# Performance work log

Measured on AMD Instinct MI355X. Metric: run time of the kernel, lower is better.

## Reference

```python
import jax, jax.numpy as jnp
import numpy as np

B = 16384
N_TABLES = 26
N_ROWS = 100000
D = 64


def _mlp(x, params, last_sigmoid=False):
    n = len(params)
    for i, (w, b) in enumerate(params):
        x = x @ w.T + b
        if last_sigmoid and i == n - 1:
            x = jax.nn.sigmoid(x)
        else:
            x = jax.nn.relu(x)
    return x


def setup_inputs() -> dict:
    key = jax.random.key(0)
    ks = jax.random.split(key, 16)

    def glorot(k, m, n):
        return jax.random.normal(k, (m, n), jnp.float32) * np.sqrt(2.0 / (m + n))

    def bias(k, m):
        return jax.random.normal(k, (m,), jnp.float32) * np.sqrt(1.0 / m)

    return {
        "dense_x": jax.random.normal(ks[0], (B, 13), jnp.float32),
        "lS_i": jax.random.randint(ks[1], (N_TABLES, B), 0, N_ROWS, jnp.int64 if jax.config.jax_enable_x64 else jnp.int32),
        "emb_W": jax.random.normal(ks[2], (N_TABLES, N_ROWS, D), jnp.float32) * np.sqrt(1.0 / N_ROWS),
        "bot_w0": glorot(ks[3], 512, 13), "bot_b0": bias(ks[4], 512),
        "bot_w1": glorot(ks[5], 256, 512), "bot_b1": bias(ks[6], 256),
        "bot_w2": glorot(ks[7], 64, 256), "bot_b2": bias(ks[8], 64),
        "top_w0": glorot(ks[9], 512, 415), "top_b0": bias(ks[10], 512),
        "top_w1": glorot(ks[11], 256, 512), "top_b1": bias(ks[12], 256),
        "top_w2": glorot(ks[13], 1, 256), "top_b2": bias(ks[14], 1),
    }


def reference(dense_x, lS_i, emb_W, bot_w0, bot_b0, bot_w1, bot_b1, bot_w2, bot_b2,
              top_w0, top_b0, top_w1, top_b1, top_w2, top_b2):
    # bottom MLP: [B,13] -> [B,64]
    x = _mlp(dense_x, [(bot_w0, bot_b0), (bot_w1, bot_b1), (bot_w2, bot_b2)])

    # embedding lookups: one index per sample per table (EmbeddingBag sum over bag of 1)
    # emb_W: [T, N, D], lS_i: [T, B] -> ly: [T, B, D]
    ly = jnp.take_along_axis(emb_W, lS_i[:, :, None], axis=1)  # [T, B, D]

    # interaction: T = concat(x, ly) -> [B, 27, D]; Z = T T^T; lower-tri (i>j) flatten
    T = jnp.concatenate([x[None], ly], axis=0).transpose(1, 0, 2)  # [B, 27, D]
    Z = jnp.einsum("bnd,bmd->bnm", T, T)  # [B, 27, 27]
    li, lj = jnp.tril_indices(N_TABLES + 1, k=-1)  # same order as torch list comp
    Zflat = Z[:, li, lj]  # [B, 351]
    R = jnp.concatenate([x, Zflat], axis=1)  # [B, 415]

    # top MLP with sigmoid output
    p = _mlp(R, [(top_w0, top_b0), (top_w1, top_b1), (top_w2, top_b2)], last_sigmoid=True)
    return p
```

## Files before the change

kernel.cpp:

```cpp
#include <hip/hip_runtime.h>
#include <math.h>


#define BATCH 16384
#define NTAB 26
#define NF 27
#define NROWS 100000
#define EDIM 64
#define PAIRS 351
#define RLD 416

typedef __attribute__((ext_vector_type(4))) float   accfrag_t;
typedef __attribute__((ext_vector_type(8))) short   bfrag_t;
typedef __attribute__((ext_vector_type(4))) unsigned short u16x4;

__device__ __forceinline__ unsigned short f32_to_bf16(float f) {
    unsigned int u = __float_as_uint(f);
    u += 0x7fffu + ((u >> 16) & 1u);
    return (unsigned short)(u >> 16);
}
__device__ __forceinline__ float bf16_to_f32(unsigned short h) {
    return __uint_as_float(((unsigned int)h) << 16);
}

__device__ __forceinline__ void gload16(const void* g, void* l) {
    __builtin_amdgcn_global_load_lds(
        (const __attribute__((address_space(1))) unsigned int*)g,
        (__attribute__((address_space(3))) unsigned int*)l, 16, 0, 0);
}

template<int BM, int BN, int EPI>
__global__ __launch_bounds__(256) void gemm_mfma_split(
    const unsigned short* __restrict__ Ah, const unsigned short* __restrict__ Al, int lda,
    const unsigned short* __restrict__ Wh, const unsigned short* __restrict__ Wl, int ldw,
    const float* __restrict__ bias,
    unsigned short* __restrict__ Chi, unsigned short* __restrict__ Clo, int ldc,
    float* __restrict__ Cf, int ldcf,
    int K)
{
    constexpr int FM = BM / 32;
    constexpr int FN = BN / 32;

    __shared__ unsigned short sAh[4 * BM * 8];
    __shared__ unsigned short sAl[4 * BM * 8];
    __shared__ unsigned short sWh[4 * BN * 8];
    __shared__ unsigned short sWl[4 * BN * 8];

    const int tid  = threadIdx.x;
    const int lane = tid & 63;
    const int wid  = tid >> 6;
    const int wr   = wid >> 1;
    const int wc   = wid & 1;
    const int lr   = lane & 15;
    const int ls   = lane >> 4;
    const int mblk = blockIdx.x * BM;
    const int nblk = blockIdx.y * BN;

    accfrag_t acc[FM][FN];
#pragma unroll
    for (int mi = 0; mi < FM; ++mi)
#pragma unroll
        for (int nj = 0; nj < FN; ++nj) acc[mi][nj] = (accfrag_t)0.f;

    const int ktiles = K >> 5;
    for (int kt = 0; kt < ktiles; ++kt) {
        const int k0 = kt * 32;
#pragma unroll
        for (int i = 0; i < (4 * BM) / 256; ++i) {
            int c = tid + i * 256;
            int slot = c / BM, row = c % BM;
            size_t go = (size_t)(mblk + row) * lda + k0 + slot * 8;
            gload16(Ah + go, &sAh[c * 8]);
            gload16(Al + go, &sAl[c * 8]);
        }
#pragma unroll
        for (int i = 0; i < (4 * BN) / 256; ++i) {
            int c = tid + i * 256;
            int slot = c / BN, row = c % BN;
            size_t go = (size_t)(nblk + row) * ldw + k0 + slot * 8;
            gload16(Wh + go, &sWh[c * 8]);
            gload16(Wl + go, &sWl[c * 8]);
        }
        __syncthreads();

        bfrag_t ah[FM], al[FM], bh[FN], bl[FN];
#pragma unroll
        for (int mi = 0; mi < FM; ++mi) {
            int r = wr * (BM / 2) + mi * 16 + lr;
            ah[mi] = *(const bfrag_t*)&sAh[(ls * BM + r) * 8];
            al[mi] = *(const bfrag_t*)&sAl[(ls * BM + r) * 8];
        }
#pragma unroll
        for (int nj = 0; nj < FN; ++nj) {
            int cidx = wc * (BN / 2) + nj * 16 + lr;
            bh[nj] = *(const bfrag_t*)&sWh[(ls * BN + cidx) * 8];
            bl[nj] = *(const bfrag_t*)&sWl[(ls * BN + cidx) * 8];
        }
#pragma unroll
        for (int mi = 0; mi < FM; ++mi)
#pragma unroll
            for (int nj = 0; nj < FN; ++nj) {
                acc[mi][nj] = __builtin_amdgcn_mfma_f32_16x16x32_bf16(ah[mi], bh[nj], acc[mi][nj], 0, 0, 0);
                acc[mi][nj] = __builtin_amdgcn_mfma_f32_16x16x32_bf16(ah[mi], bl[nj], acc[mi][nj], 0, 0, 0);
                acc[mi][nj] = __builtin_amdgcn_mfma_f32_16x16x32_bf16(al[mi], bh[nj], acc[mi][nj], 0, 0, 0);
            }
        __syncthreads();
    }

    float bs[FN];
#pragma unroll
    for (int nj = 0; nj < FN; ++nj)
        bs[nj] = bias[nblk + wc * (BN / 2) + nj * 16 + lr];

#pragma unroll
    for (int mi = 0; mi < FM; ++mi)
#pragma unroll
        for (int nj = 0; nj < FN; ++nj) {
            int col = nblk + wc * (BN / 2) + nj * 16 + lr;
#pragma unroll
            for (int j = 0; j < 4; ++j) {
                int row = mblk + wr * (BM / 2) + mi * 16 + ls * 4 + j;
                float v = acc[mi][nj][j] + bs[nj];
                v = v > 0.f ? v : 0.f;
                if (EPI == 0 || EPI == 1) {
                    unsigned short h = f32_to_bf16(v);
                    Chi[(size_t)row * ldc + col] = h;
                    Clo[(size_t)row * ldc + col] = f32_to_bf16(v - bf16_to_f32(h));
                }
                if (EPI == 1 || EPI == 2) {
                    Cf[(size_t)row * ldcf + col] = v;
                }
            }
        }
}

__global__ __launch_bounds__(256) void decomp_w_kernel(
    const float* __restrict__ w, unsigned short* __restrict__ hi,
    unsigned short* __restrict__ lo, int N, int Kin, int Kout)
{
    int idx = blockIdx.x * 256 + threadIdx.x;
    if (idx >= N * Kout) return;
    int n = idx / Kout, k = idx - n * Kout;
    float v = (k < Kin) ? w[(size_t)n * Kin + k] : 0.f;
    unsigned short h = f32_to_bf16(v);
    hi[idx] = h;
    lo[idx] = f32_to_bf16(v - bf16_to_f32(h));
}

__global__ __launch_bounds__(256) void bot0_kernel(
    const float* __restrict__ x,
    const float* __restrict__ w0,
    const float* __restrict__ b0,
    unsigned short* __restrict__ oh, unsigned short* __restrict__ ol)
{
    __shared__ float Wt[13][512];
    __shared__ float xs[2][13];
    __shared__ float bsh[512];
    const int tid = threadIdx.x;
    for (int i = tid; i < 13 * 512; i += 256) {
        int n = i / 13, k = i - n * 13;
        Wt[k][n] = w0[i];
    }
    bsh[tid] = b0[tid];
    bsh[tid + 256] = b0[tid + 256];
    const int brow0 = blockIdx.x * 2;
    if (tid < 26) xs[tid / 13][tid % 13] = x[(size_t)brow0 * 13 + tid];
    __syncthreads();

    const int bl = tid >> 7;
    const int n0 = (tid & 127) * 4;
    const int b  = brow0 + bl;
    float a0 = bsh[n0], a1 = bsh[n0 + 1], a2 = bsh[n0 + 2], a3 = bsh[n0 + 3];
#pragma unroll
    for (int k = 0; k < 13; ++k) {
        float xv = xs[bl][k];
        float4 wv = *(const float4*)&Wt[k][n0];
        a0 += xv * wv.x; a1 += xv * wv.y; a2 += xv * wv.z; a3 += xv * wv.w;
    }
    a0 = fmaxf(a0, 0.f); a1 = fmaxf(a1, 0.f); a2 = fmaxf(a2, 0.f); a3 = fmaxf(a3, 0.f);
    u16x4 h, l;
    h.x = f32_to_bf16(a0); l.x = f32_to_bf16(a0 - bf16_to_f32(h.x));
    h.y = f32_to_bf16(a1); l.y = f32_to_bf16(a1 - bf16_to_f32(h.y));
    h.z = f32_to_bf16(a2); l.z = f32_to_bf16(a2 - bf16_to_f32(h.z));
    h.w = f32_to_bf16(a3); l.w = f32_to_bf16(a3 - bf16_to_f32(h.w));
    *(u16x4*)&oh[(size_t)b * 512 + n0] = h;
    *(u16x4*)&ol[(size_t)b * 512 + n0] = l;
}

__global__ __launch_bounds__(256) void interact_kernel(
    const float* __restrict__ emb,
    const int*   __restrict__ lsi,
    const float* __restrict__ xf,
    unsigned short* __restrict__ Rhi, unsigned short* __restrict__ Rlo)
{
    __shared__ float Tl[4][NF][68];
    const int wave = threadIdx.x >> 6;
    const int lane = threadIdx.x & 63;
    const int b = blockIdx.x * 4 + wave;

    Tl[wave][0][lane] = xf[(size_t)b * EDIM + lane];
#pragma unroll 2
    for (int t = 0; t < NTAB; ++t) {
        int row = lsi[t * BATCH + b];
        Tl[wave][t + 1][lane] = emb[((size_t)t * NROWS + row) * EDIM + lane];
    }
    __syncthreads();

    for (int p = lane; p < PAIRS; p += 64) {
        int i = (int)((1.0f + sqrtf(1.0f + 8.0f * (float)p)) * 0.5f);
        while (i * (i - 1) / 2 > p) --i;
        while ((i + 1) * i / 2 <= p) ++i;
        int j = p - i * (i - 1) / 2;

        const float4* ri = (const float4*)&Tl[wave][i][0];
        const float4* rj = (const float4*)&Tl[wave][j][0];
        float s = 0.f;
#pragma unroll
        for (int d = 0; d < EDIM / 4; ++d) {
            float4 a = ri[d], c = rj[d];
            s += a.x * c.x + a.y * c.y + a.z * c.z + a.w * c.w;
        }
        size_t o = (size_t)b * RLD + EDIM + p;
        unsigned short h = f32_to_bf16(s);
        Rhi[o] = h;
        Rlo[o] = f32_to_bf16(s - bf16_to_f32(h));
    }
    if (lane == 0) {
        size_t o = (size_t)b * RLD + 415;
        Rhi[o] = 0;
        Rlo[o] = 0;
    }
}

__global__ __launch_bounds__(256) void top_final_kernel(
    const float* __restrict__ h,
    const float* __restrict__ w,
    const float* __restrict__ bias,
    float* __restrict__ out)
{
    const int wave = threadIdx.x >> 6;
    const int lane = threadIdx.x & 63;
    const int b = blockIdx.x * 4 + wave;

    const float4* hv = (const float4*)&h[(size_t)b * 256];
    const float4* wv = (const float4*)w;
    float4 a = hv[lane];
    float4 c = wv[lane];
    float s = a.x * c.x + a.y * c.y + a.z * c.z + a.w * c.w;
#pragma unroll
    for (int off = 32; off; off >>= 1) s += __shfl_down(s, off);
    if (lane == 0) {
        float z = s + bias[0];
        out[b] = 1.f / (1.f + expf(-z));
    }
}

extern "C" void kernel_launch(void* const* d_in, const int* in_sizes, int n_in,
                              void* d_out, int out_size, void* d_ws, size_t ws_size,
                              hipStream_t stream)
{
    const float* dense_x = (const float*)d_in[0];
    const int*   lS_i    = (const int*)  d_in[1];
    const float* emb_W   = (const float*)d_in[2];
    const float* bot_w0  = (const float*)d_in[3];
    const float* bot_b0  = (const float*)d_in[4];
    const float* bot_w1  = (const float*)d_in[5];
    const float* bot_b1  = (const float*)d_in[6];
    const float* bot_w2  = (const float*)d_in[7];
    const float* bot_b2  = (const float*)d_in[8];
    const float* top_w0  = (const float*)d_in[9];
    const float* top_b0  = (const float*)d_in[10];
    const float* top_w1  = (const float*)d_in[11];
    const float* top_b1  = (const float*)d_in[12];
    const float* top_w2  = (const float*)d_in[13];
    const float* top_b2  = (const float*)d_in[14];
    float* out = (float*)d_out;

    unsigned short* p = (unsigned short*)d_ws;
    unsigned short* hAhi = p; p += (size_t)BATCH * 512;
    unsigned short* hAlo = p; p += (size_t)BATCH * 512;
    unsigned short* hBhi = p; p += (size_t)BATCH * 256;
    unsigned short* hBlo = p; p += (size_t)BATCH * 256;
    unsigned short* Rhi  = p; p += (size_t)BATCH * RLD;
    unsigned short* Rlo  = p; p += (size_t)BATCH * RLD;
    float* xf  = (float*)p;
    float* hBf = xf + (size_t)BATCH * EDIM;
    unsigned short* q = (unsigned short*)(hBf + (size_t)BATCH * 256);
    unsigned short* w1h = q; q += 256 * 512;
    unsigned short* w1l = q; q += 256 * 512;
    unsigned short* w2h = q; q += 64 * 256;
    unsigned short* w2l = q; q += 64 * 256;
    unsigned short* t0h = q; q += 512 * RLD;
    unsigned short* t0l = q; q += 512 * RLD;
    unsigned short* t1h = q; q += 256 * 512;
    unsigned short* t1l = q; q += 256 * 512;

    dim3 blk(256);

    decomp_w_kernel<<<dim3((256 * 512 + 255) / 256), blk, 0, stream>>>(bot_w1, w1h, w1l, 256, 512, 512);
    decomp_w_kernel<<<dim3((64 * 256 + 255) / 256), blk, 0, stream>>>(bot_w2, w2h, w2l, 64, 256, 256);
    decomp_w_kernel<<<dim3((512 * RLD + 255) / 256), blk, 0, stream>>>(top_w0, t0h, t0l, 512, 415, RLD);
    decomp_w_kernel<<<dim3((256 * 512 + 255) / 256), blk, 0, stream>>>(top_w1, t1h, t1l, 256, 512, 512);

    bot0_kernel<<<dim3(BATCH / 2), blk, 0, stream>>>(dense_x, bot_w0, bot_b0, hAhi, hAlo);
    gemm_mfma_split<64, 128, 0><<<dim3(BATCH / 64, 256 / 128), blk, 0, stream>>>(
        hAhi, hAlo, 512, w1h, w1l, 512, bot_b1, hBhi, hBlo, 256, nullptr, 0, 512);
    gemm_mfma_split<64, 64, 1><<<dim3(BATCH / 64, 1), blk, 0, stream>>>(
        hBhi, hBlo, 256, w2h, w2l, 256, bot_b2, Rhi, Rlo, RLD, xf, EDIM, 256);

    interact_kernel<<<dim3(BATCH / 4), blk, 0, stream>>>(emb_W, lS_i, xf, Rhi, Rlo);

    gemm_mfma_split<64, 128, 0><<<dim3(BATCH / 64, 512 / 128), blk, 0, stream>>>(
        Rhi, Rlo, RLD, t0h, t0l, RLD, top_b0, hAhi, hAlo, 512, nullptr, 0, RLD);
    gemm_mfma_split<64, 128, 2><<<dim3(BATCH / 64, 256 / 128), blk, 0, stream>>>(
        hAhi, hAlo, 512, t1h, t1l, 512, top_b1, nullptr, nullptr, 0, hBf, 256, 512);
    top_final_kernel<<<dim3(BATCH / 4), blk, 0, stream>>>(hBf, top_w2, top_b2, out);
}
```

Baseline: 967.0 us.

## Fuse final linear+sigmoid into top GEMM, merge decompositions, MFMA bottom layer

The final 256->1 dot product and sigmoid move into the epilogue of the last top-MLP GEMM, which now covers all 256 columns per block and reduces across lanes through shared memory. This removes the float intermediate write and the separate kernel. All weight and input bf16 hi/lo splits are merged into a single launch, and the first bottom layer (K=13, zero-padded to 32) now runs on the MFMA GEMM instead of a scalar kernel. The cost is extra work on padded K and a wider BN=256 tile, which means more accumulator registers and only 256 blocks for the last GEMM.

```diff
diff --git a/kernel.cpp b/kernel.cpp
--- a/kernel.cpp
+++ b/kernel.cpp
@@ -9,10 +9,10 @@
 #define EDIM 64
 #define PAIRS 351
 #define RLD 416
-
-typedef __attribute__((ext_vector_type(4))) float   accfrag_t;
-typedef __attribute__((ext_vector_type(8))) short   bfrag_t;
-typedef __attribute__((ext_vector_type(4))) unsigned short u16x4;
+#define XK 32
+
+typedef __attribute__((ext_vector_type(4))) float accfrag_t;
+typedef __attribute__((ext_vector_type(8))) short bfrag_t;
 
 __device__ __forceinline__ unsigned short f32_to_bf16(float f) {
     unsigned int u = __float_as_uint(f);
@@ -36,6 +36,8 @@
     const float* __restrict__ bias,
     unsigned short* __restrict__ Chi, unsigned short* __restrict__ Clo, int ldc,
     float* __restrict__ Cf, int ldcf,
+    const float* __restrict__ wfin, const float* __restrict__ bfin,
+    float* __restrict__ outp,
     int K)
 {
     constexpr int FM = BM / 32;
@@ -112,79 +114,112 @@
     for (int nj = 0; nj < FN; ++nj)
         bs[nj] = bias[nblk + wc * (BN / 2) + nj * 16 + lr];
 
-#pragma unroll
-    for (int mi = 0; mi < FM; ++mi)
-#pragma unroll
-        for (int nj = 0; nj < FN; ++nj) {
-            int col = nblk + wc * (BN / 2) + nj * 16 + lr;
+    if constexpr (EPI == 3) {
+        __shared__ float red[BM][2];
+        float wv[FN];
+#pragma unroll
+        for (int nj = 0; nj < FN; ++nj)
+            wv[nj] = wfin[wc * (BN / 2) + nj * 16 + lr];
+#pragma unroll
+        for (int mi = 0; mi < FM; ++mi)
 #pragma unroll
             for (int j = 0; j < 4; ++j) {
-                int row = mblk + wr * (BM / 2) + mi * 16 + ls * 4 + j;
-                float v = acc[mi][nj][j] + bs[nj];
-                v = v > 0.f ? v : 0.f;
-                if (EPI == 0 || EPI == 1) {
+                float part = 0.f;
+#pragma unroll
+                for (int nj = 0; nj < FN; ++nj) {
+                    float v = acc[mi][nj][j] + bs[nj];
+                    v = v > 0.f ? v : 0.f;
+                    part += v * wv[nj];
+                }
+#pragma unroll
+                for (int off = 1; off < 16; off <<= 1)
+                    part += __shfl_xor(part, off);
+                if (lr == 0)
+                    red[wr * (BM / 2) + mi * 16 + ls * 4 + j][wc] = part;
+            }
+        __syncthreads();
+        if (tid < BM) {
+            float s = red[tid][0] + red[tid][1] + bfin[0];
+            outp[mblk + tid] = 1.f / (1.f + expf(-s));
+        }
+    } else {
+#pragma unroll
+        for (int mi = 0; mi < FM; ++mi)
+#pragma unroll
+            for (int nj = 0; nj < FN; ++nj) {
+                int col = nblk + wc * (BN / 2) + nj * 16 + lr;
+#pragma unroll
+                for (int j = 0; j < 4; ++j) {
+                    int row = mblk + wr * (BM / 2) + mi * 16 + ls * 4 + j;
+                    float v = acc[mi][nj][j] + bs[nj];
+                    v = v > 0.f ? v : 0.f;
                     unsigned short h = f32_to_bf16(v);
                     Chi[(size_t)row * ldc + col] = h;
                     Clo[(size_t)row * ldc + col] = f32_to_bf16(v - bf16_to_f32(h));
-                }
-                if (EPI == 1 || EPI == 2) {
-                    Cf[(size_t)row * ldcf + col] = v;
+                    if (EPI == 1) Cf[(size_t)row * ldcf + col] = v;
                 }
             }
-        }
-}
-
-__global__ __launch_bounds__(256) void decomp_w_kernel(
-    const float* __restrict__ w, unsigned short* __restrict__ hi,
-    unsigned short* __restrict__ lo, int N, int Kin, int Kout)
+    }
+}
+
+#define XB_   2048
+#define W0B_  64
+#define W1B_  512
+#define W2B_  64
+#define T0B_  832
+#define T1B_  512
+
+__global__ __launch_bounds__(256) void decomp_all(
+    const float* __restrict__ x,
+    const float* __restrict__ w0,
+    const float* __restrict__ w1,
+    const float* __restrict__ w2,
+    const float* __restrict__ t0,
+    const float* __restrict__ t1,
+    unsigned short* __restrict__ xh,  unsigned short* __restrict__ xl,
+    unsigned short* __restrict__ w0h, unsigned short* __restrict__ w0l,
+    unsigned short* __restrict__ w1h, unsigned short* __restrict__ w1l,
+    unsigned short* __restrict__ w2h, unsigned short* __restrict__ w2l,
+    unsigned short* __restrict__ t0h, unsigned short* __restrict__ t0l,
+    unsigned short* __restrict__ t1h, unsigned short* __restrict__ t1l)
 {
-    int idx = blockIdx.x * 256 + threadIdx.x;
-    if (idx >= N * Kout) return;
-    int n = idx / Kout, k = idx - n * Kout;
-    float v = (k < Kin) ? w[(size_t)n * Kin + k] : 0.f;
+    const int blk = blockIdx.x;
+    const int t = threadIdx.x;
+    float v;
+    unsigned short* hi;
+    unsigned short* lo;
+    int idx;
+    if (blk < XB_) {
+        idx = blk * 256 + t;
+        int b = idx >> 5, k = idx & 31;
+        v = (k < 13) ? x[b * 13 + k] : 0.f;
+        hi = xh; lo = xl;
+    } else if (blk < XB_ + W0B_) {
+        idx = (blk - XB_) * 256 + t;
+        int n = idx >> 5, k = idx & 31;
+        v = (k < 13) ? w0[n * 13 + k] : 0.f;
+        hi = w0h; lo = w0l;
+    } else if (blk < XB_ + W0B_ + W1B_) {
+        idx = (blk - XB_ - W0B_) * 256 + t;
+        v = w1[idx];
+        hi = w1h; lo = w1l;
+    } else if (blk < XB_ + W0B_ + W1B_ + W2B_) {
+        idx = (blk - XB_ - W0B_ - W1B_) * 256 + t;
+        v = w2[idx];
+        hi = w2h; lo = w2l;
+    } else if (blk < XB_ + W0B_ + W1B_ + W2B_ + T0B_) {
+        idx = (blk - XB_ - W0B_ - W1B_ - W2B_) * 256 + t;
+        int n = idx / RLD, k = idx - n * RLD;
+        v = (k < 415) ? t0[n * 415 + k] : 0.f;
+        hi = t0h; lo = t0l;
+    } else {
+        idx = (blk - XB_ - W0B_ - W1B_ - W2B_ - T0B_) * 256 + t;
+        v = t1[idx];
+        hi = t1h; lo = t1l;
+    }
     unsigned short h = f32_to_bf16(v);
     hi[idx] = h;
     lo[idx] = f32_to_bf16(v - bf16_to_f32(h));
-}
-
-__global__ __launch_bounds__(256) void bot0_kernel(
-    const float* __restrict__ x,
-    const float* __restrict__ w0,
-    const float* __restrict__ b0,
-    unsigned short* __restrict__ oh, unsigned short* __restrict__ ol)
-{
-    __shared__ float Wt[13][512];
-    __shared__ float xs[2][13];
-    __shared__ float bsh[512];
-    const int tid = threadIdx.x;
-    for (int i = tid; i < 13 * 512; i += 256) {
-        int n = i / 13, k = i - n * 13;
-        Wt[k][n] = w0[i];
-    }
-    bsh[tid] = b0[tid];
-    bsh[tid + 256] = b0[tid + 256];
-    const int brow0 = blockIdx.x * 2;
-    if (tid < 26) xs[tid / 13][tid % 13] = x[(size_t)brow0 * 13 + tid];
-    __syncthreads();
-
-    const int bl = tid >> 7;
-    const int n0 = (tid & 127) * 4;
-    const int b  = brow0 + bl;
-    float a0 = bsh[n0], a1 = bsh[n0 + 1], a2 = bsh[n0 + 2], a3 = bsh[n0 + 3];
-#pragma unroll
-    for (int k = 0; k < 13; ++k) {
-        float xv = xs[bl][k];
-        float4 wv = *(const float4*)&Wt[k][n0];
-        a0 += xv * wv.x; a1 += xv * wv.y; a2 += xv * wv.z; a3 += xv * wv.w;
-    }
-    a0 = fmaxf(a0, 0.f); a1 = fmaxf(a1, 0.f); a2 = fmaxf(a2, 0.f); a3 = fmaxf(a3, 0.f);
-    u16x4 h, l;
-    h.x = f32_to_bf16(a0); l.x = f32_to_bf16(a0 - bf16_to_f32(h.x));
-    h.y = f32_to_bf16(a1); l.y = f32_to_bf16(a1 - bf16_to_f32(h.y));
-    h.z = f32_to_bf16(a2); l.z = f32_to_bf16(a2 - bf16_to_f32(h.z));
-    h.w = f32_to_bf16(a3); l.w = f32_to_bf16(a3 - bf16_to_f32(h.w));
-    *(u16x4*)&oh[(size_t)b * 512 + n0] = h;
-    *(u16x4*)&ol[(size_t)b * 512 + n0] = l;
 }
 
 __global__ __launch_bounds__(256) void interact_kernel(
@@ -229,29 +264,6 @@
         size_t o = (size_t)b * RLD + 415;
         Rhi[o] = 0;
         Rlo[o] = 0;
-    }
-}
-
-__global__ __launch_bounds__(256) void top_final_kernel(
-    const float* __restrict__ h,
-    const float* __restrict__ w,
-    const float* __restrict__ bias,
-    float* __restrict__ out)
-{
-    const int wave = threadIdx.x >> 6;
-    const int lane = threadIdx.x & 63;
-    const int b = blockIdx.x * 4 + wave;
-
-    const float4* hv = (const float4*)&h[(size_t)b * 256];
-    const float4* wv = (const float4*)w;
-    float4 a = hv[lane];
-    float4 c = wv[lane];
-    float s = a.x * c.x + a.y * c.y + a.z * c.z + a.w * c.w;
-#pragma unroll
-    for (int off = 32; off; off >>= 1) s += __shfl_down(s, off);
-    if (lane == 0) {
-        float z = s + bias[0];
-        out[b] = 1.f / (1.f + expf(-z));
     }
 }
 
@@ -276,43 +288,52 @@
     const float* top_b2  = (const float*)d_in[14];
     float* out = (float*)d_out;
 
-    unsigned short* p = (unsigned short*)d_ws;
+    float* xf = (float*)d_ws;
+    unsigned short* p = (unsigned short*)(xf + (size_t)BATCH * EDIM);
     unsigned short* hAhi = p; p += (size_t)BATCH * 512;
     unsigned short* hAlo = p; p += (size_t)BATCH * 512;
     unsigned short* hBhi = p; p += (size_t)BATCH * 256;
     unsigned short* hBlo = p; p += (size_t)BATCH * 256;
     unsigned short* Rhi  = p; p += (size_t)BATCH * RLD;
     unsigned short* Rlo  = p; p += (size_t)BATCH * RLD;
-    float* xf  = (float*)p;
-    float* hBf = xf + (size_t)BATCH * EDIM;
-    unsigned short* q = (unsigned short*)(hBf + (size_t)BATCH * 256);
-    unsigned short* w1h = q; q += 256 * 512;
-    unsigned short* w1l = q; q += 256 * 512;
-    unsigned short* w2h = q; q += 64 * 256;
-    unsigned short* w2l = q; q += 64 * 256;
-    unsigned short* t0h = q; q += 512 * RLD;
-    unsigned short* t0l = q; q += 512 * RLD;
-    unsigned short* t1h = q; q += 256 * 512;
-    unsigned short* t1l = q; q += 256 * 512;
+    unsigned short* xh   = p; p += (size_t)BATCH * XK;
+    unsigned short* xl   = p; p += (size_t)BATCH * XK;
+    unsigned short* w0h  = p; p += 512 * XK;
+    unsigned short* w0l  = p; p += 512 * XK;
+    unsigned short* w1h  = p; p += 256 * 512;
+    unsigned short* w1l  = p; p += 256 * 512;
+    unsigned short* w2h  = p; p += 64 * 256;
+    unsigned short* w2l  = p; p += 64 * 256;
+    unsigned short* t0h  = p; p += 512 * RLD;
+    unsigned short* t0l  = p; p += 512 * RLD;
+    unsigned short* t1h  = p; p += 256 * 512;
+    unsigned short* t1l  = p; p += 256 * 512;
 
     dim3 blk(256);
 
-    decomp_w_kernel<<<dim3((256 * 512 + 255) / 256), blk, 0, stream>>>(bot_w1, w1h, w1l, 256, 512, 512);
-    decomp_w_kernel<<<dim3((64 * 256 + 255) / 256), blk, 0, stream>>>(bot_w2, w2h, w2l, 64, 256, 256);
-    decomp_w_kernel<<<dim3((512 * RLD + 255) / 256), blk, 0, stream>>>(top_w0, t0h, t0l, 512, 415, RLD);
-    decomp_w_kernel<<<dim3((256 * 512 + 255) / 256), blk, 0, stream>>>(top_w1, t1h, t1l, 256, 512, 512);
-
-    bot0_kernel<<<dim3(BATCH / 2), blk, 0, stream>>>(dense_x, bot_w0, bot_b0, hAhi, hAlo);
+    decomp_all<<<dim3(XB_ + W0B_ + W1B_ + W2B_ + T0B_ + T1B_), blk, 0, stream>>>(
+        dense_x, bot_w0, bot_w1, bot_w2, top_w0, top_w1,
+        xh, xl, w0h, w0l, w1h, w1l, w2h, w2l, t0h, t0l, t1h, t1l);
+
+    gemm_mfma_split<64, 128, 0><<<dim3(BATCH / 64, 512 / 128), blk, 0, stream>>>(
+        xh, xl, XK, w0h, w0l, XK, bot_b0, hAhi, hAlo, 512,
+        nullptr, 0, nullptr, nullptr, nullptr, XK);
+
     gemm_mfma_split<64, 128, 0><<<dim3(BATCH / 64, 256 / 128), blk, 0, stream>>>(
-        hAhi, hAlo, 512, w1h, w1l, 512, bot_b1, hBhi, hBlo, 256, nullptr, 0, 512);
+        hAhi, hAlo, 512, w1h, w1l, 512, bot_b1, hBhi, hBlo, 256,
+        nullptr, 0, nullptr, nullptr, nullptr, 512);
+
     gemm_mfma_split<64, 64, 1><<<dim3(BATCH / 64, 1), blk, 0, stream>>>(
-        hBhi, hBlo, 256, w2h, w2l, 256, bot_b2, Rhi, Rlo, RLD, xf, EDIM, 256);
+        hBhi, hBlo, 256, w2h, w2l, 256, bot_b2, Rhi, Rlo, RLD,
+        xf, EDIM, nullptr, nullptr, nullptr, 256);
 
     interact_kernel<<<dim3(BATCH / 4), blk, 0, stream>>>(emb_W, lS_i, xf, Rhi, Rlo);
 
     gemm_mfma_split<64, 128, 0><<<dim3(BATCH / 64, 512 / 128), blk, 0, stream>>>(
-        Rhi, Rlo, RLD, t0h, t0l, RLD, top_b0, hAhi, hAlo, 512, nullptr, 0, RLD);
-    gemm_mfma_split<64, 128, 2><<<dim3(BATCH / 64, 256 / 128), blk, 0, stream>>>(
-        hAhi, hAlo, 512, t1h, t1l, 512, top_b1, nullptr, nullptr, 0, hBf, 256, 512);
-    top_final_kernel<<<dim3(BATCH / 4), blk, 0, stream>>>(hBf, top_w2, top_b2, out);
-}
+        Rhi, Rlo, RLD, t0h, t0l, RLD, top_b0, hAhi, hAlo, 512,
+        nullptr, 0, nullptr, nullptr, nullptr, RLD);
+
+    gemm_mfma_split<64, 256, 3><<<dim3(BATCH / 64, 1), blk, 0, stream>>>(
+        hAhi, hAlo, 512, t1h, t1l, 512, top_b1, nullptr, nullptr, 0,
+        nullptr, 0, top_w2, top_b2, out, 512);
+}
```

Measured after the change: 942.5 us. -2.5%, faster.
